# Kernel tuning notes

Measured on AMD Instinct MI355X. Metric: run time of the kernel, lower is better.

The kernel has to match this reference:

```python
import jax, jax.numpy as jnp
import numpy as np

N = 8192        # points
M = 131072      # query-key pairs (edges)
C_IN = 512
H = 8           # heads
D = 64          # head_channels
BINS = 48
BIN_SIZE = 0.05


def setup_inputs() -> dict:
    key = jax.random.key(0)
    ks = jax.random.split(key, 8)
    x_F = jax.random.normal(ks[0], (N, C_IN), dtype=jnp.float32)
    x_C = jax.random.uniform(ks[1], (N, 3), dtype=jnp.float32)
    qk_pair_idxs = jax.random.randint(ks[2], (2, M), 0, N, dtype=jnp.int64)
    W_qkv = jax.random.normal(ks[3], (C_IN, 3 * H * D), dtype=jnp.float32) * 0.02
    b_qkv = jnp.zeros((3 * H * D,), dtype=jnp.float32)
    q_tables = jax.random.normal(ks[4], (3, BINS, H, D), dtype=jnp.float32) * 0.02
    k_tables = jax.random.normal(ks[5], (3, BINS, H, D), dtype=jnp.float32) * 0.02
    v_tables = jax.random.normal(ks[6], (3, BINS, H, D), dtype=jnp.float32) * 0.02
    return {"x_F": x_F, "x_C": x_C, "qk_pair_idxs": qk_pair_idxs,
            "W_qkv": W_qkv, "b_qkv": b_qkv,
            "q_tables": q_tables, "k_tables": k_tables, "v_tables": v_tables}


def reference(x_F, x_C, qk_pair_idxs, W_qkv, b_qkv, q_tables, k_tables, v_tables):
    n = x_F.shape[0]
    qkv = (x_F @ W_qkv + b_qkv).reshape(n, 3, H, D)
    q = qkv[:, 0] * (D ** -0.5)   # scale folded into queries, as in the module
    k = qkv[:, 1]
    v = qkv[:, 2]
    qi = qk_pair_idxs[0]
    ki = qk_pair_idxs[1]
    # quantized relative coordinates -> table bin indices [M,3]
    rel = (x_C[qi] - x_C[ki]) / BIN_SIZE + BINS / 2
    idx = jnp.clip(rel.astype(jnp.int32), 0, BINS - 1)
    # precompute per-point, per-axis, per-bin table dot products [N,3,BINS,H]
    q_dot = jnp.einsum('nhd,abhd->nabh', q, q_tables)
    k_dot = jnp.einsum('nhd,abhd->nabh', k, k_tables)
    # content logits [M,H]
    logits = jnp.einsum('mhd,mhd->mh', q[qi], k[ki])
    for a in range(3):  # fixed xyz axes
        logits = logits + q_dot[qi, a, idx[:, a]] + k_dot[ki, a, idx[:, a]]
    # scatter softmax over query index (per head)
    seg_max = jax.ops.segment_max(logits, qi, num_segments=n)
    e = jnp.exp(logits - seg_max[qi])
    denom = jax.ops.segment_sum(e, qi, num_segments=n)
    attn = e / denom[qi]  # [M,H]
    # value-side relative position bias, summed over axes [M,H,D]
    vt = v_tables[0, idx[:, 0]] + v_tables[1, idx[:, 1]] + v_tables[2, idx[:, 2]]
    contrib = attn[:, :, None] * (v[ki] + vt)            # [M,H,D]
    agg = jax.ops.segment_sum(contrib, qi, num_segments=n)  # [N,H,D]
    return agg.reshape(n, H * D)
```

## Files before the change

kernel.cpp:

```cpp
#include <hip/hip_runtime.h>
#include <hip/hip_bf16.h>
#include <stdint.h>

#define N_PTS 8192
#define M_EDGES 131072
#define CIN 512
#define QKV_COLS 1536

typedef __bf16 bf16x8 __attribute__((ext_vector_type(8)));
typedef float f32x4 __attribute__((ext_vector_type(4)));

#define GAS __attribute__((address_space(1)))
#define LAS __attribute__((address_space(3)))

__device__ __forceinline__ void gload_lds16(const void* g, void* l) {
  __builtin_amdgcn_global_load_lds((const GAS void*)g, (LAS void*)l, 16, 0, 0);
}

__global__ __launch_bounds__(256) void prep_kernel(
    const float* __restrict__ xF, const float* __restrict__ W,
    const float* __restrict__ qt, const float* __restrict__ kt,
    const float* __restrict__ vt, const int* __restrict__ pairs,
    const float* __restrict__ xc,
    __bf16* __restrict__ A, __bf16* __restrict__ BT,
    __bf16* __restrict__ qtb, __bf16* __restrict__ ktb, __bf16* __restrict__ vtT,
    int* __restrict__ qi_a, unsigned* __restrict__ pack0, int* __restrict__ cnt) {
  __shared__ float tile[32][33];
  int b = blockIdx.x;
  int tid = threadIdx.x;
  if (b < 4096) {
    int base = (b * 256 + tid) * 4;
    float4 v = *(const float4*)(xF + base);
    A[base + 0] = (__bf16)v.x;
    A[base + 1] = (__bf16)v.y;
    A[base + 2] = (__bf16)v.z;
    A[base + 3] = (__bf16)v.w;
  } else if (b < 4864) {
    int blk = b - 4096;
    int bk = blk & 15, bn = blk >> 4;
    int x = tid & 31, y = tid >> 5;
#pragma unroll
    for (int j = 0; j < 4; j++) {
      int r = y + j * 8;
      tile[r][x] = W[(size_t)(bk * 32 + r) * QKV_COLS + bn * 32 + x];
    }
    __syncthreads();
#pragma unroll
    for (int j = 0; j < 4; j++) {
      int r = y + j * 8;
      BT[(size_t)(bn * 32 + r) * CIN + bk * 32 + x] = (__bf16)tile[x][r];
    }
  } else if (b < 5152) {
    int i = (b - 4864) * 256 + tid;
    int d = i & 63, h = (i >> 6) & 7, ab = i >> 9;
    int po = (h * 144 + ab) * 64 + d;
    qtb[po] = (__bf16)qt[i];
    ktb[po] = (__bf16)kt[i];
  } else if (b < 5472) {
    int i = (b - 5152) * 256 + tid;
    int p = i % 160;
    int d = (i / 160) & 63;
    int h = i / 10240;
    vtT[i] = (p < 144) ? (__bf16)vt[p * 512 + h * 64 + d] : (__bf16)0.f;
  } else {
    int m = (b - 5472) * 256 + tid;
    int qi = pairs[m], ki = pairs[M_EDGES + m];
    unsigned pb = 0;
#pragma unroll
    for (int a = 0; a < 3; a++) {
      float rel = (xc[qi * 3 + a] - xc[ki * 3 + a]) / 0.05f + 24.0f;
      int bb = (int)rel;
      bb = bb < 0 ? 0 : (bb > 47 ? 47 : bb);
      pb |= (unsigned)bb << (6 * a);
    }
    qi_a[m] = qi;
    pack0[m] = (unsigned)ki | (pb << 13);
    atomicAdd(&cnt[qi], 1);
  }
}

__global__ __launch_bounds__(256) void gemm_scan_kernel(
    const __bf16* __restrict__ A, const __bf16* __restrict__ BT,
    const float* __restrict__ bias, __bf16* __restrict__ qb,
    __bf16* __restrict__ kv,
    const int* __restrict__ cnt, int* __restrict__ off, int* __restrict__ cursor) {
  __shared__ __align__(16) char At[2][64 * 128];
  __shared__ __align__(16) char Bt[2][128 * 128];
  __shared__ int wsum[4];
  int bid = blockIdx.x;
  int tid = threadIdx.x;

  if (bid == 1536) {
    int lane = tid & 63, w = tid >> 6;
    int local[32];
    int s = 0;
#pragma unroll
    for (int i = 0; i < 8; i++) {
      int4 v = ((const int4*)cnt)[tid * 8 + i];
      local[i * 4 + 0] = v.x; local[i * 4 + 1] = v.y;
      local[i * 4 + 2] = v.z; local[i * 4 + 3] = v.w;
      s += v.x + v.y + v.z + v.w;
    }
    int incl = s;
#pragma unroll
    for (int d = 1; d < 64; d <<= 1) {
      int t = __shfl_up(incl, d, 64);
      if (lane >= d) incl += t;
    }
    if (lane == 63) wsum[w] = incl;
    __syncthreads();
    int woff = 0;
#pragma unroll
    for (int j = 0; j < 4; j++) woff += (j < w) ? wsum[j] : 0;
    int run = woff + incl - s;
    int base = tid * 32;
#pragma unroll
    for (int i = 0; i < 32; i++) {
      off[base + i] = run;
      cursor[base + i] = run;
      run += local[i];
    }
    if (tid == 255) off[N_PTS] = run;
    return;
  }

  int bn = bid % 12, bm = bid / 12;
  int w = tid >> 6, l = tid & 63;
  int wm = w & 1, wn = w >> 1;
  f32x4 acc[2][4] = {};
  const char* Ab = (const char*)A;
  const char* Bb = (const char*)BT;
  int lr = l & 15;
  int lk = (l >> 4) * 16;
  int xr = (lr & 7) << 4;

  auto stage = [&](int tk, int buf) {
#pragma unroll
    for (int r = 0; r < 2; r++) {
      int flat = r * 4096 + tid * 16;
      int row = flat >> 7, colb = flat & 127;
      int gcolb = colb ^ ((row & 7) << 4);
      gload_lds16(Ab + ((size_t)(bm * 64 + row) * CIN + tk * 64) * 2 + gcolb,
                  At[buf] + r * 4096 + w * 1024);
    }
#pragma unroll
    for (int r = 0; r < 4; r++) {
      int flat = r * 4096 + tid * 16;
      int row = flat >> 7, colb = flat & 127;
      int gcolb = colb ^ ((row & 7) << 4);
      gload_lds16(Bb + ((size_t)(bn * 128 + row) * CIN + tk * 64) * 2 + gcolb,
                  Bt[buf] + r * 4096 + w * 1024);
    }
  };

  stage(0, 0);
  __syncthreads();
  int cur = 0;
  for (int kt = 0; kt < 8; kt++) {
    if (kt < 7) stage(kt + 1, cur ^ 1);
#pragma unroll
    for (int ks = 0; ks < 2; ks++) {
      bf16x8 af[2], bfr[4];
      int cs = (ks * 64 + lk) ^ xr;
#pragma unroll
      for (int mf = 0; mf < 2; mf++) af[mf] = *(const bf16x8*)(At[cur] + (wm * 32 + mf * 16 + lr) * 128 + cs);
#pragma unroll
      for (int nf = 0; nf < 4; nf++) bfr[nf] = *(const bf16x8*)(Bt[cur] + (wn * 64 + nf * 16 + lr) * 128 + cs);
#pragma unroll
      for (int mf = 0; mf < 2; mf++)
#pragma unroll
        for (int nf = 0; nf < 4; nf++)
          acc[mf][nf] = __builtin_amdgcn_mfma_f32_16x16x32_bf16(af[mf], bfr[nf], acc[mf][nf], 0, 0, 0);
    }
    __syncthreads();
    cur ^= 1;
  }

  int lg = l >> 4;
#pragma unroll
  for (int mf = 0; mf < 2; mf++) {
#pragma unroll
    for (int nf = 0; nf < 4; nf++) {
      int gc = bn * 128 + wn * 64 + nf * 16 + lr;
      float b = bias[gc];
      int which = gc >> 9;
      int col = gc & 511;
      float scale = which == 0 ? 0.125f : 1.0f;
#pragma unroll
      for (int j = 0; j < 4; j++) {
        int gr = bm * 64 + wm * 32 + mf * 16 + lg * 4 + j;
        float val = (acc[mf][nf][j] + b) * scale;
        if (which == 0) qb[(size_t)gr * 512 + col] = (__bf16)val;
        else kv[(size_t)gr * 1024 + (which == 2 ? 512 : 0) + col] = (__bf16)val;
      }
    }
  }
}

__global__ __launch_bounds__(256) void table_dot(const __bf16* __restrict__ qb,
                                                 const __bf16* __restrict__ kv,
                                                 const __bf16* __restrict__ qtb,
                                                 const __bf16* __restrict__ ktb,
                                                 __bf16* __restrict__ qdot,
                                                 __bf16* __restrict__ kdot) {
  __shared__ __align__(16) char As[128 * 128];
  __shared__ __align__(16) char Bs[144 * 128];
  int nt = blockIdx.x, h = blockIdx.y, z = blockIdx.z;
  const __bf16* src = z ? kv : qb;
  const __bf16* tab = z ? ktb : qtb;
  __bf16* out = z ? kdot : qdot;
  size_t SB = z ? 2048 : 1024;
  int tid = threadIdx.x, w = tid >> 6, l = tid & 63;
  const char* sb = (const char*)src;
  const char* tb = (const char*)tab + (size_t)h * 144 * 128;
#pragma unroll
  for (int p = 0; p < 4; p++) {
    int flat = p * 4096 + tid * 16;
    int row = flat >> 7, colb = flat & 127;
    int gcolb = colb ^ ((row & 7) << 4);
    gload_lds16(sb + (size_t)(nt * 128 + row) * SB + h * 128 + gcolb, As + p * 4096 + w * 1024);
    gload_lds16(tb + row * 128 + gcolb, Bs + p * 4096 + w * 1024);
  }
  if (w < 2) {
    int flat = 16384 + w * 1024 + l * 16;
    int row = flat >> 7, colb = flat & 127;
    int gcolb = colb ^ ((row & 7) << 4);
    gload_lds16(tb + row * 128 + gcolb, Bs + 16384 + w * 1024);
  }
  __syncthreads();

  f32x4 acc[2][9] = {};
  int lr = l & 15, lk = (l >> 4) * 16;
  int xr = (lr & 7) << 4;
#pragma unroll
  for (int ks = 0; ks < 2; ks++) {
    bf16x8 af[2], bf[9];
    int cs = (ks * 64 + lk) ^ xr;
#pragma unroll
    for (int mf = 0; mf < 2; mf++)
      af[mf] = *(const bf16x8*)(As + (w * 32 + mf * 16 + lr) * 128 + cs);
#pragma unroll
    for (int nf = 0; nf < 9; nf++)
      bf[nf] = *(const bf16x8*)(Bs + (nf * 16 + lr) * 128 + cs);
#pragma unroll
    for (int mf = 0; mf < 2; mf++)
#pragma unroll
      for (int nf = 0; nf < 9; nf++)
        acc[mf][nf] = __builtin_amdgcn_mfma_f32_16x16x32_bf16(af[mf], bf[nf], acc[mf][nf], 0, 0, 0);
  }

  int lg = l >> 4;
#pragma unroll
  for (int mf = 0; mf < 2; mf++)
#pragma unroll
    for (int nf = 0; nf < 9; nf++)
#pragma unroll
      for (int j = 0; j < 4; j++) {
        int n = nt * 128 + w * 32 + mf * 16 + lg * 4 + j;
        int ab = nf * 16 + lr;
        out[(size_t)n * 1152 + ab * 8 + h] = (__bf16)acc[mf][nf][j];
      }
}

__global__ void scatter_k(const int* __restrict__ qi_a, const unsigned* __restrict__ pack0,
                          const __bf16* __restrict__ kdot, int* __restrict__ cursor,
                          unsigned* __restrict__ epack, __bf16* __restrict__ khat) {
  int m = blockIdx.x * blockDim.x + threadIdx.x;
  if (m >= M_EDGES) return;
  int qi = qi_a[m];
  unsigned pk = pack0[m];
  int pos = atomicAdd(&cursor[qi], 1);
  epack[pos] = pk;
  int ki = pk & 8191;
  unsigned pb = pk >> 13;
  const __bf16* kd = kdot + (size_t)ki * 1152;
  bf16x8 t0 = *(const bf16x8*)(kd + ((pb & 63u)) * 8);
  bf16x8 t1 = *(const bf16x8*)(kd + (48 + ((pb >> 6) & 63u)) * 8);
  bf16x8 t2 = *(const bf16x8*)(kd + (96 + ((pb >> 12) & 63u)) * 8);
  bf16x8 o;
#pragma unroll
  for (int j = 0; j < 8; j++)
    o[j] = (__bf16)((float)t0[j] + (float)t1[j] + (float)t2[j]);
  *(bf16x8*)(khat + ((size_t)pos << 3)) = o;
}

__global__ __launch_bounds__(256) void attn_kernel(
    const __bf16* __restrict__ qb, const __bf16* __restrict__ kv,
    const __bf16* __restrict__ qdot, const __bf16* __restrict__ khat,
    const int* __restrict__ off, const unsigned* __restrict__ epack,
    float* __restrict__ num, float* __restrict__ den, __bf16* __restrict__ Hb) {
  __shared__ float hist[8 * 164];
  __shared__ float part[4][512];
  __shared__ float dpart[4][8];
  int n = blockIdx.x;
  int tid = threadIdx.x;
  int w = tid >> 6, l = tid & 63;
  int h = l >> 3, dg = l & 7;

  for (int i = tid; i < 8 * 164; i += 256) hist[i] = 0.f;
  __syncthreads();

  bf16x8 q8 = *(const bf16x8*)(qb + (n << 9) + l * 8);
  float qv[8];
#pragma unroll
  for (int j = 0; j < 8; j++) qv[j] = (float)q8[j];

  float acc[8] = {0.f, 0.f, 0.f, 0.f, 0.f, 0.f, 0.f, 0.f};
  float dn = 0.f;
  int e0 = off[n], e1 = off[n + 1];
  const __bf16* qd_row = qdot + (size_t)n * 1152;

  for (int e = e0 + w; e < e1; e += 4) {
    unsigned pk = epack[__builtin_amdgcn_readfirstlane(e)];
    int ki = pk & 8191;
    unsigned pb = pk >> 13;
    bf16x8 k8 = *(const bf16x8*)(kv + ((size_t)ki << 10) + l * 8);
    bf16x8 v8 = *(const bf16x8*)(kv + ((size_t)ki << 10) + 512 + l * 8);
    float p;
    if (dg < 3) {
      int bin = (int)((pb >> (6 * dg)) & 63u);
      p = (float)qd_row[(dg * 48 + bin) * 8 + h];
    } else if (dg == 3) {
      p = (float)khat[((size_t)e << 3) + h];
    } else {
      p = 0.f;
    }
#pragma unroll
    for (int j = 0; j < 8; j++) p += qv[j] * (float)k8[j];
    p += __shfl_xor(p, 1, 64);
    p += __shfl_xor(p, 2, 64);
    p += __shfl_xor(p, 4, 64);
    float x = __expf(p);
    dn += x;
#pragma unroll
    for (int j = 0; j < 8; j++) acc[j] += x * (float)v8[j];
    if (dg == 0) {
      float* hh = hist + h * 164;
      atomicAdd(hh + (pb & 63), x);
      atomicAdd(hh + 48 + ((pb >> 6) & 63), x);
      atomicAdd(hh + 96 + ((pb >> 12) & 63), x);
    }
  }

  f32x4 a0 = {acc[0], acc[1], acc[2], acc[3]};
  f32x4 a1 = {acc[4], acc[5], acc[6], acc[7]};
  *(f32x4*)&part[w][l * 8] = a0;
  *(f32x4*)&part[w][l * 8 + 4] = a1;
  if (dg == 0) dpart[w][h] = dn;
  __syncthreads();

#pragma unroll
  for (int half = 0; half < 2; half++) {
    int idx = tid + half * 256;
    float s = 0.f;
#pragma unroll
    for (int ww = 0; ww < 4; ww++) s += part[ww][idx];
    num[(n << 9) + idx] = s;
  }
  if (tid < 8) {
    float d = 0.f;
#pragma unroll
    for (int ww = 0; ww < 4; ww++) d += dpart[ww][tid];
    den[n * 8 + tid] = d;
  }
  for (int i = tid; i < 1280; i += 256) {
    int hh = i / 160, p = i % 160;
    Hb[(size_t)n * 1280 + i] = (__bf16)hist[hh * 164 + p];
  }
}

__global__ __launch_bounds__(256) void finish_kernel(const __bf16* __restrict__ Hb,
                                                     const __bf16* __restrict__ vtT,
                                                     const float* __restrict__ den,
                                                     float* __restrict__ out) {
  __shared__ __align__(16) char As[2][128 * 64];
  __shared__ __align__(16) char Bs[2][64 * 64];
  int nt = blockIdx.x, h = blockIdx.y;
  int tid = threadIdx.x, w = tid >> 6, l = tid & 63;
  int lr = l & 15, lk = (l >> 4) * 16;
  int xr = (lr & 3) << 4;
  const char* Ab = (const char*)Hb;
  const char* Bb = (const char*)vtT;
  f32x4 acc[2][4] = {};

  auto stage = [&](int tk, int buf) {
#pragma unroll
    for (int c = 0; c < 2; c++) {
      int flat = c * 4096 + tid * 16;
      int row = flat >> 6, colb = flat & 63;
      int gcolb = colb ^ ((row & 3) << 4);
      gload_lds16(Ab + ((size_t)(nt * 128 + row) * 1280 + h * 160 + tk * 32) * 2 + gcolb,
                  As[buf] + c * 4096 + w * 1024);
    }
    {
      int flat = tid * 16;
      int row = flat >> 6, colb = flat & 63;
      int gcolb = colb ^ ((row & 3) << 4);
      gload_lds16(Bb + ((size_t)(h * 64 + row) * 160 + tk * 32) * 2 + gcolb,
                  Bs[buf] + w * 1024);
    }
  };

  stage(0, 0);
  __syncthreads();
  int cur = 0;
  for (int kt = 0; kt < 5; kt++) {
    if (kt < 4) stage(kt + 1, cur ^ 1);
    bf16x8 af[2], bf[4];
    int cs = lk ^ xr;
#pragma unroll
    for (int mf = 0; mf < 2; mf++) af[mf] = *(const bf16x8*)(As[cur] + (w * 32 + mf * 16 + lr) * 64 + cs);
#pragma unroll
    for (int nf = 0; nf < 4; nf++) bf[nf] = *(const bf16x8*)(Bs[cur] + (nf * 16 + lr) * 64 + cs);
#pragma unroll
    for (int mf = 0; mf < 2; mf++)
#pragma unroll
      for (int nf = 0; nf < 4; nf++)
        acc[mf][nf] = __builtin_amdgcn_mfma_f32_16x16x32_bf16(af[mf], bf[nf], acc[mf][nf], 0, 0, 0);
    __syncthreads();
    cur ^= 1;
  }

  int lg = l >> 4;
#pragma unroll
  for (int mf = 0; mf < 2; mf++) {
#pragma unroll
    for (int j = 0; j < 4; j++) {
      int n = nt * 128 + w * 32 + mf * 16 + lg * 4 + j;
      float dnv = den[n * 8 + h];
      float inv = dnv > 0.f ? 1.f / dnv : 0.f;
#pragma unroll
      for (int nf = 0; nf < 4; nf++) {
        int gi = (n << 9) + h * 64 + nf * 16 + lr;
        out[gi] = (out[gi] + acc[mf][nf][j]) * inv;
      }
    }
  }
}

extern "C" void kernel_launch(void* const* d_in, const int* in_sizes, int n_in,
                              void* d_out, int out_size, void* d_ws, size_t ws_size,
                              hipStream_t stream) {
  const float* xF = (const float*)d_in[0];
  const float* xC = (const float*)d_in[1];
  const int* pairs = (const int*)d_in[2];
  const float* W = (const float*)d_in[3];
  const float* bias = (const float*)d_in[4];
  const float* qt = (const float*)d_in[5];
  const float* kt = (const float*)d_in[6];
  const float* vt = (const float*)d_in[7];
  float* out = (float*)d_out;

  char* ws = (char*)d_ws;
  size_t o = 0;
  auto alloc = [&](size_t bytes) {
    void* p = ws + o;
    o = (o + bytes + 255) & ~(size_t)255;
    return p;
  };
  char* region0 = (char*)alloc((size_t)N_PTS * 1280 * 2);
  __bf16* A = (__bf16*)region0;
  __bf16* BT = (__bf16*)(region0 + (size_t)N_PTS * CIN * 2);
  __bf16* Hb = (__bf16*)region0;
  __bf16* qb = (__bf16*)alloc((size_t)N_PTS * 512 * 2);
  __bf16* kv = (__bf16*)alloc((size_t)N_PTS * 1024 * 2);
  __bf16* qtb = (__bf16*)alloc((size_t)8 * 144 * 64 * 2);
  __bf16* ktb = (__bf16*)alloc((size_t)8 * 144 * 64 * 2);
  __bf16* vtT = (__bf16*)alloc((size_t)8 * 64 * 160 * 2);
  __bf16* qdot = (__bf16*)alloc((size_t)N_PTS * 1152 * 2);
  __bf16* kdot = (__bf16*)alloc((size_t)N_PTS * 1152 * 2);
  __bf16* khat = (__bf16*)alloc((size_t)M_EDGES * 8 * 2);
  float* den = (float*)alloc((size_t)N_PTS * 8 * 4);
  int* qi_a = (int*)alloc(M_EDGES * 4);
  unsigned* pack0 = (unsigned*)alloc(M_EDGES * 4);
  unsigned* epack = (unsigned*)alloc(M_EDGES * 4);
  int* cnt = (int*)alloc(N_PTS * 4);
  int* off = (int*)alloc((N_PTS + 1) * 4);
  int* cursor = (int*)alloc(N_PTS * 4);

  hipMemsetAsync(cnt, 0, N_PTS * 4, stream);

  prep_kernel<<<5984, 256, 0, stream>>>(xF, W, qt, kt, vt, pairs, xC,
                                        A, BT, qtb, ktb, vtT, qi_a, pack0, cnt);
  gemm_scan_kernel<<<1537, 256, 0, stream>>>(A, BT, bias, qb, kv, cnt, off, cursor);
  table_dot<<<dim3(N_PTS / 128, 8, 2), 256, 0, stream>>>(qb, kv, qtb, ktb, qdot, kdot);
  scatter_k<<<M_EDGES / 256, 256, 0, stream>>>(qi_a, pack0, kdot, cursor, epack, khat);
  attn_kernel<<<N_PTS, 256, 0, stream>>>(qb, kv, qdot, khat, off, epack, out, den, Hb);
  finish_kernel<<<dim3(N_PTS / 128, 8), 256, 0, stream>>>(Hb, vtT, den, out);
}
```

Measured before the change: 153.3 us.

## Merge edge scatter into table-dot kernel and gather k-bias directly in attention

The edge bucketing scatter now runs as extra blocks inside the table-dot kernel, which removes one launch and lets the two independent jobs overlap. The per-edge precomputed khat array (three kdot gathers summed per edge) is dropped. Instead, lanes dg 3-5 in the attention kernel gather their own axis's kdot entry, and the existing shuffle reduction sums it with the rest. This avoids writing and re-reading khat. The cost is more scattered kdot reads inside the attention loop, and the bias is now summed in fp32 rather than pre-rounded to bf16.

Result: no change. 151.4 us (-1.2%).

```diff
diff --git a/kernel.cpp b/kernel.cpp
--- a/kernel.cpp
+++ b/kernel.cpp
@@ -197,20 +197,32 @@
   }
 }
 
-__global__ __launch_bounds__(256) void table_dot(const __bf16* __restrict__ qb,
-                                                 const __bf16* __restrict__ kv,
-                                                 const __bf16* __restrict__ qtb,
-                                                 const __bf16* __restrict__ ktb,
-                                                 __bf16* __restrict__ qdot,
-                                                 __bf16* __restrict__ kdot) {
+__global__ __launch_bounds__(256) void td_scatter_kernel(
+    const __bf16* __restrict__ qb, const __bf16* __restrict__ kv,
+    const __bf16* __restrict__ qtb, const __bf16* __restrict__ ktb,
+    __bf16* __restrict__ qdot, __bf16* __restrict__ kdot,
+    const int* __restrict__ qi_a, const unsigned* __restrict__ pack0,
+    int* __restrict__ cursor, unsigned* __restrict__ epack) {
   __shared__ __align__(16) char As[128 * 128];
   __shared__ __align__(16) char Bs[144 * 128];
-  int nt = blockIdx.x, h = blockIdx.y, z = blockIdx.z;
+  int bid = blockIdx.x;
+  int tid = threadIdx.x;
+
+  if (bid < 512) {
+    int m = bid * 256 + tid;
+    int qi = qi_a[m];
+    int pos = atomicAdd(&cursor[qi], 1);
+    epack[pos] = pack0[m];
+    return;
+  }
+
+  int td = bid - 512;
+  int nt = td & 63, h = (td >> 6) & 7, z = td >> 9;
   const __bf16* src = z ? kv : qb;
   const __bf16* tab = z ? ktb : qtb;
   __bf16* out = z ? kdot : qdot;
   size_t SB = z ? 2048 : 1024;
-  int tid = threadIdx.x, w = tid >> 6, l = tid & 63;
+  int w = tid >> 6, l = tid & 63;
   const char* sb = (const char*)src;
   const char* tb = (const char*)tab + (size_t)h * 144 * 128;
 #pragma unroll
@@ -262,31 +274,9 @@
       }
 }
 
-__global__ void scatter_k(const int* __restrict__ qi_a, const unsigned* __restrict__ pack0,
-                          const __bf16* __restrict__ kdot, int* __restrict__ cursor,
-                          unsigned* __restrict__ epack, __bf16* __restrict__ khat) {
-  int m = blockIdx.x * blockDim.x + threadIdx.x;
-  if (m >= M_EDGES) return;
-  int qi = qi_a[m];
-  unsigned pk = pack0[m];
-  int pos = atomicAdd(&cursor[qi], 1);
-  epack[pos] = pk;
-  int ki = pk & 8191;
-  unsigned pb = pk >> 13;
-  const __bf16* kd = kdot + (size_t)ki * 1152;
-  bf16x8 t0 = *(const bf16x8*)(kd + ((pb & 63u)) * 8);
-  bf16x8 t1 = *(const bf16x8*)(kd + (48 + ((pb >> 6) & 63u)) * 8);
-  bf16x8 t2 = *(const bf16x8*)(kd + (96 + ((pb >> 12) & 63u)) * 8);
-  bf16x8 o;
-#pragma unroll
-  for (int j = 0; j < 8; j++)
-    o[j] = (__bf16)((float)t0[j] + (float)t1[j] + (float)t2[j]);
-  *(bf16x8*)(khat + ((size_t)pos << 3)) = o;
-}
-
 __global__ __launch_bounds__(256) void attn_kernel(
     const __bf16* __restrict__ qb, const __bf16* __restrict__ kv,
-    const __bf16* __restrict__ qdot, const __bf16* __restrict__ khat,
+    const __bf16* __restrict__ qdot, const __bf16* __restrict__ kdot,
     const int* __restrict__ off, const unsigned* __restrict__ epack,
     float* __restrict__ num, float* __restrict__ den, __bf16* __restrict__ Hb) {
   __shared__ float hist[8 * 164];
@@ -309,6 +299,8 @@
   float dn = 0.f;
   int e0 = off[n], e1 = off[n + 1];
   const __bf16* qd_row = qdot + (size_t)n * 1152;
+  int axis = dg < 3 ? dg : dg - 3;
+  int tsh = 6 * axis;
 
   for (int e = e0 + w; e < e1; e += 4) {
     unsigned pk = epack[__builtin_amdgcn_readfirstlane(e)];
@@ -316,15 +308,10 @@
     unsigned pb = pk >> 13;
     bf16x8 k8 = *(const bf16x8*)(kv + ((size_t)ki << 10) + l * 8);
     bf16x8 v8 = *(const bf16x8*)(kv + ((size_t)ki << 10) + 512 + l * 8);
-    float p;
-    if (dg < 3) {
-      int bin = (int)((pb >> (6 * dg)) & 63u);
-      p = (float)qd_row[(dg * 48 + bin) * 8 + h];
-    } else if (dg == 3) {
-      p = (float)khat[((size_t)e << 3) + h];
-    } else {
-      p = 0.f;
-    }
+    int bin = (int)((pb >> tsh) & 63u);
+    int idx = (axis * 48 + bin) * 8 + h;
+    const __bf16* tbl = dg < 3 ? qd_row : (kdot + (size_t)ki * 1152);
+    float p = (dg < 6) ? (float)tbl[idx] : 0.f;
 #pragma unroll
     for (int j = 0; j < 8; j++) p += qv[j] * (float)k8[j];
     p += __shfl_xor(p, 1, 64);
@@ -469,7 +456,6 @@
   __bf16* vtT = (__bf16*)alloc((size_t)8 * 64 * 160 * 2);
   __bf16* qdot = (__bf16*)alloc((size_t)N_PTS * 1152 * 2);
   __bf16* kdot = (__bf16*)alloc((size_t)N_PTS * 1152 * 2);
-  __bf16* khat = (__bf16*)alloc((size_t)M_EDGES * 8 * 2);
   float* den = (float*)alloc((size_t)N_PTS * 8 * 4);
   int* qi_a = (int*)alloc(M_EDGES * 4);
   unsigned* pack0 = (unsigned*)alloc(M_EDGES * 4);
@@ -483,8 +469,8 @@
   prep_kernel<<<5984, 256, 0, stream>>>(xF, W, qt, kt, vt, pairs, xC,
                                         A, BT, qtb, ktb, vtT, qi_a, pack0, cnt);
   gemm_scan_kernel<<<1537, 256, 0, stream>>>(A, BT, bias, qb, kv, cnt, off, cursor);
-  table_dot<<<dim3(N_PTS / 128, 8, 2), 256, 0, stream>>>(qb, kv, qtb, ktb, qdot, kdot);
-  scatter_k<<<M_EDGES / 256, 256, 0, stream>>>(qi_a, pack0, kdot, cursor, epack, khat);
-  attn_kernel<<<N_PTS, 256, 0, stream>>>(qb, kv, qdot, khat, off, epack, out, den, Hb);
+  td_scatter_kernel<<<1536, 256, 0, stream>>>(qb, kv, qtb, ktb, qdot, kdot,
+                                              qi_a, pack0, cursor, epack);
+  attn_kernel<<<N_PTS, 256, 0, stream>>>(qb, kv, qdot, kdot, off, epack, out, den, Hb);
   finish_kernel<<<dim3(N_PTS / 128, 8), 256, 0, stream>>>(Hb, vtT, den, out);
 }
```
